# Kernel tuning notes

Measured on AMD Instinct MI355X. Metric: run time of the kernel, lower is better.

The kernel has to match this reference:

```python
import jax, jax.numpy as jnp
import numpy as np

B, S, T = 32, 32, 64          # docs, sentences/doc, tokens/sentence
E, HW, HS = 128, 128, 128     # embed, word hidden, sentence hidden
CW, CS = 128, 128             # attention context sizes
V, NC = 50000, 8              # vocab, classes


def setup_inputs() -> dict:
    key = jax.random.key(0)
    ks = iter(jax.random.split(key, 40))
    x = jax.random.randint(next(ks), (B, S, T), 1, V, dtype=jnp.int32)
    wl = jax.random.randint(next(ks), (B, S), 8, T + 1)   # word lengths
    sl = jax.random.randint(next(ks), (B,), 8, S + 1)     # sentence counts
    tmask = jnp.arange(T)[None, None, :] < wl[:, :, None]
    smask = (jnp.arange(S)[None, :] < sl[:, None])[:, :, None]
    x = jnp.where(tmask & smask, x, 0)                     # 0 = pad token

    def u(shape, scale=0.1):
        return jax.random.uniform(next(ks), shape, jnp.float32, -scale, scale)

    d = {"x": x, "emb": u((V, E))}
    # GRU params in torch layout: W_ih [3H,D] (r|z|n), W_hh [3H,H], biases [3H]
    for pre, Din, H in [("wf", E, HW), ("wb", E, HW), ("sf", 2 * HW, HS), ("sb", 2 * HW, HS)]:
        d[pre + "_Wih"] = u((3 * H, Din))
        d[pre + "_Whh"] = u((3 * H, H))
        d[pre + "_bih"] = u((3 * H,))
        d[pre + "_bhh"] = u((3 * H,))
    d["wproj_W"] = u((CW, 2 * HW)); d["wproj_b"] = u((CW,)); d["wctx"] = u((CW,))
    d["sproj_W"] = u((CS, 2 * HS)); d["sproj_b"] = u((CS,)); d["sctx"] = u((CS,))
    d["fc_W"] = u((NC, 2 * HS)); d["fc_b"] = u((NC,))
    return d


def seq_lens_2d(tok):
    # torch get_sequence_lens: T - trailing zeros, 1 if all zero
    nz = tok != 0
    any_nz = jnp.any(nz, axis=1)
    last = tok.shape[1] - jnp.argmax(nz[:, ::-1], axis=1)
    return jnp.where(any_nz, last, 1)


def doc_lens(x):
    # torch get_num_sentences_lens: S - trailing all-zero sentences
    nz = jnp.any(x != 0, axis=2)  # [B,S]
    any_nz = jnp.any(nz, axis=1)
    last = x.shape[1] - jnp.argmax(nz[:, ::-1], axis=1)
    return jnp.where(any_nz, last, 1)


def run_gru(x, lens, Wih, Whh, bih, bhh, reverse):
    # x: [N,Tm,D]; emulates pack_padded: state frozen / output zeroed beyond len
    N, Tm, _ = x.shape
    H = Whh.shape[1]
    xp = jnp.einsum('ntd,gd->ntg', x, Wih) + bih  # [N,Tm,3H]

    def step(h, inp):
        xg, t = inp
        hg = h @ Whh.T + bhh
        xr, xz, xn = jnp.split(xg, 3, axis=-1)
        hr, hz, hn = jnp.split(hg, 3, axis=-1)
        r = jax.nn.sigmoid(xr + hr)
        z = jax.nn.sigmoid(xz + hz)
        n = jnp.tanh(xn + r * hn)
        h_new = (1 - z) * n + z * h
        valid = (t < lens)[:, None]
        h_new = jnp.where(valid, h_new, h)
        return h_new, jnp.where(valid, h_new, 0.0)

    h0 = jnp.zeros((N, H), x.dtype)
    _, ys = jax.lax.scan(step, h0, (jnp.swapaxes(xp, 0, 1), jnp.arange(Tm)), reverse=reverse)
    return jnp.swapaxes(ys, 0, 1)  # [N,Tm,H]


def bigru(x, lens, pf, pb):
    return jnp.concatenate([run_gru(x, lens, *pf, reverse=False),
                            run_gru(x, lens, *pb, reverse=True)], axis=-1)


def attn_pool(out, lens, Wp, bp, ctx):
    # faithful to torch: softmax over padded positions up to max(lens)
    # (pad_packed pads to max length; padded outputs are zero but score=tanh(b)@c)
    Tm = out.shape[1]
    scores = jnp.tanh(out @ Wp.T + bp) @ ctx            # [N,Tm]
    valid = jnp.arange(Tm)[None, :] < jnp.max(lens)
    attn = jax.nn.softmax(jnp.where(valid, scores, -jnp.inf), axis=-1)
    return jnp.einsum('nt,nth->nh', attn, out)


def han_forward(x, emb,
                wf_Wih, wf_Whh, wf_bih, wf_bhh, wb_Wih, wb_Whh, wb_bih, wb_bhh,
                wproj_W, wproj_b, wctx,
                sf_Wih, sf_Whh, sf_bih, sf_bhh, sb_Wih, sb_Whh, sb_bih, sb_bhh,
                sproj_W, sproj_b, sctx, fc_W, fc_b):
    Bx, Sx, Tx = x.shape
    xw = x.reshape(-1, Tx)                      # [B*S, T]
    wlens = seq_lens_2d(xw)
    slens = doc_lens(x)
    we = emb[xw]                                # [B*S, T, E]
    wout = bigru(we, wlens, (wf_Wih, wf_Whh, wf_bih, wf_bhh),
                 (wb_Wih, wb_Whh, wb_bih, wb_bhh))     # [B*S, T, 2HW]
    sent = attn_pool(wout, wlens, wproj_W, wproj_b, wctx)  # [B*S, 2HW]
    sent = sent.reshape(Bx, Sx, -1)
    sout = bigru(sent, slens, (sf_Wih, sf_Whh, sf_bih, sf_bhh),
                 (sb_Wih, sb_Whh, sb_bih, sb_bhh))     # [B, S, 2HS]
    doc = attn_pool(sout, slens, sproj_W, sproj_b, sctx)   # [B, 2HS]
    return doc @ fc_W.T + fc_b                             # [B, NC]


def reference(x, emb,
              wf_Wih, wf_Whh, wf_bih, wf_bhh, wb_Wih, wb_Whh, wb_bih, wb_bhh,
              wproj_W, wproj_b, wctx,
              sf_Wih, sf_Whh, sf_bih, sf_bhh, sb_Wih, sb_Whh, sb_bih, sb_bhh,
              sproj_W, sproj_b, sctx, fc_W, fc_b):
    return han_forward(x, emb,
                       wf_Wih, wf_Whh, wf_bih, wf_bhh, wb_Wih, wb_Whh, wb_bih, wb_bhh,
                       wproj_W, wproj_b, wctx,
                       sf_Wih, sf_Whh, sf_bih, sf_bhh, sb_Wih, sb_Whh, sb_bih, sb_bhh,
                       sproj_W, sproj_b, sctx, fc_W, fc_b)
```

## Files before the change

kernel.cpp:

```cpp
#include <hip/hip_runtime.h>
#include <hip/hip_bf16.h>

typedef unsigned short ushort_t;
typedef __attribute__((ext_vector_type(4))) float floatx4;
typedef __attribute__((ext_vector_type(8))) short short8;

__device__ __forceinline__ float bf2f(ushort_t u) {
    union { unsigned int i; float f; } v; v.i = ((unsigned int)u) << 16; return v.f;
}
__device__ __forceinline__ ushort_t f2bf(float f) {
    union { float f; unsigned int i; } v; v.f = f;
    unsigned int i = v.i;
    i += 0x7fffu + ((i >> 16) & 1u);
    return (ushort_t)(i >> 16);
}
__device__ __forceinline__ float fsig(float x)  { return 1.f / (1.f + __expf(-x)); }
__device__ __forceinline__ float ftanh(float x) { return 1.f - 2.f / (__expf(2.f * x) + 1.f); }

__device__ __forceinline__ floatx4 MFMA16(short8 a, short8 b, floatx4 c) {
    return __builtin_amdgcn_mfma_f32_16x16x32_bf16(a, b, c, 0, 0, 0);
}

#define XIDX(c, m) ((((c) * 16) + ((m) ^ ((c) & 15))) * 8)

__global__ __launch_bounds__(64) void detect_kernel(const unsigned int* __restrict__ raw,
                                                    int* __restrict__ flag,
                                                    int* __restrict__ wmax,
                                                    int* __restrict__ smax) {
    int c = 0;
    for (int i = 0; i < 16; ++i) {
        unsigned int v = raw[threadIdx.x * 16 + i];
        unsigned int e = (v >> 7) & 0xFFu;
        if (e > 0x7Bu) ++c;
    }
    c += __shfl_xor(c, 1);  c += __shfl_xor(c, 2);  c += __shfl_xor(c, 4);
    c += __shfl_xor(c, 8);  c += __shfl_xor(c, 16); c += __shfl_xor(c, 32);
    if (threadIdx.x == 0) {
        *flag = (c > 64) ? 1 : 0;
        *wmax = 0;
        *smax = 0;
    }
}

struct ConvArgs {
    const void* src[25];
    int dstoff[25];
    int count[25];
    int cumblk[26];
};

__global__ __launch_bounds__(256) void convert_kernel(ConvArgs a, ushort_t* __restrict__ dst,
                                                      const int* __restrict__ flag) {
    int b = blockIdx.x;
    int lo = 0, hi = 24;
    while (lo < hi) { int mid = (lo + hi + 1) >> 1; if (a.cumblk[mid] <= b) lo = mid; else hi = mid - 1; }
    int j = lo;
    size_t base = (size_t)(b - a.cumblk[j]) * 2048 + (size_t)threadIdx.x * 8;
    if (base >= (size_t)a.count[j]) return;
    ushort_t* out = dst + a.dstoff[j] + base;
    if (*flag) {
        const float* s = (const float*)a.src[j] + base;
        float4 v0 = *(const float4*)s;
        float4 v1 = *(const float4*)(s + 4);
        union { ushort_t u[8]; uint4 v; } o;
        o.u[0] = f2bf(v0.x); o.u[1] = f2bf(v0.y); o.u[2] = f2bf(v0.z); o.u[3] = f2bf(v0.w);
        o.u[4] = f2bf(v1.x); o.u[5] = f2bf(v1.y); o.u[6] = f2bf(v1.z); o.u[7] = f2bf(v1.w);
        *(uint4*)out = o.v;
    } else {
        *(uint4*)out = *(const uint4*)((const ushort_t*)a.src[j] + base);
    }
}

__global__ __launch_bounds__(64) void lens_kernel(const int* __restrict__ x,
                                                  int* wlens, int* slens,
                                                  int* wmax, int* smax) {
    int b = blockIdx.x, s = threadIdx.x;
    int last = 0;
    if (s < 32) {
        const int* tok = x + (b * 32 + s) * 64;
        for (int t = 0; t < 64; t += 4) {
            int4 v = *(const int4*)(tok + t);
            if (v.x) last = t + 1;
            if (v.y) last = t + 2;
            if (v.z) last = t + 3;
            if (v.w) last = t + 4;
        }
        wlens[b * 32 + s] = last ? last : 1;
    }
    int len = (s < 32) ? (last ? last : 1) : 0;
    int lm = len;
    for (int off = 32; off; off >>= 1) lm = max(lm, __shfl_xor(lm, off));
    unsigned long long mask = __ballot(s < 32 && last > 0);
    if (s == 0) {
        int sl = mask ? (63 - (int)__clzll(mask) + 1) : 1;
        slens[b] = sl;
        atomicMax(smax, sl);
        atomicMax(wmax, lm);
    }
}

__global__ __launch_bounds__(512, 2) void word_gru_kernel(
        const int* __restrict__ x, const ushort_t* __restrict__ emb,
        const ushort_t* __restrict__ Wih_f, const ushort_t* __restrict__ Whh_f,
        const ushort_t* __restrict__ bih_f, const ushort_t* __restrict__ bhh_f,
        const ushort_t* __restrict__ Wih_b, const ushort_t* __restrict__ Whh_b,
        const ushort_t* __restrict__ bih_b, const ushort_t* __restrict__ bhh_b,
        const int* __restrict__ lens, ushort_t* __restrict__ out) {
    const int T = 64;
    __shared__ ushort_t h_buf[2][2048];
    __shared__ ushort_t x_buf[2][2048];
    __shared__ float bsum_lds[256];
    __shared__ float bihn_lds[128];
    __shared__ float bhhn_lds[128];
    __shared__ int tok_lds[1024];

    int tid = threadIdx.x;
    int d = blockIdx.y;
    int n0 = blockIdx.x * 16;
    const ushort_t* Wih = d ? Wih_b : Wih_f;
    const ushort_t* Whh = d ? Whh_b : Whh_f;
    const ushort_t* bih = d ? bih_b : bih_f;
    const ushort_t* bhh = d ? bhh_b : bhh_f;
    int lane = tid & 63, wave = tid >> 6;
    int l15 = lane & 15, l4 = (lane >> 4) & 3;
    int jt = wave * 16;
    int j0 = jt + l4 * 4;

    ((int2*)tok_lds)[tid] = ((const int2*)(x + n0 * 64))[tid];
    if (tid < 256) bsum_lds[tid] = bf2f(bih[tid]) + bf2f(bhh[tid]);
    else if (tid < 384) {
        bihn_lds[tid - 256] = bf2f(bih[tid]);
        bhhn_lds[tid - 256] = bf2f(bhh[tid]);
    }
    { uint2 z = {0u, 0u}; *(uint2*)&h_buf[0][tid * 4] = z; }

    short8 wr[4], wz[4], wn[4], ur[4], uz[4], un[4];
    #pragma unroll
    for (int kf = 0; kf < 4; ++kf) {
        int col = kf * 32 + l4 * 8;
        wr[kf] = *(const short8*)(Wih + (size_t)(jt + l15) * 128 + col);
        wz[kf] = *(const short8*)(Wih + (size_t)(128 + jt + l15) * 128 + col);
        wn[kf] = *(const short8*)(Wih + (size_t)(256 + jt + l15) * 128 + col);
        ur[kf] = *(const short8*)(Whh + (size_t)(jt + l15) * 128 + col);
        uz[kf] = *(const short8*)(Whh + (size_t)(128 + jt + l15) * 128 + col);
        un[kf] = *(const short8*)(Whh + (size_t)(256 + jt + l15) * 128 + col);
    }
    __syncthreads();

    floatx4 br  = *(floatx4*)&bsum_lds[j0];
    floatx4 bz  = *(floatx4*)&bsum_lds[128 + j0];
    floatx4 bxn = *(floatx4*)&bihn_lds[j0];
    floatx4 bhn = *(floatx4*)&bhhn_lds[j0];
    int lv = lens[n0 + l15];
    float hreg[4] = {0.f, 0.f, 0.f, 0.f};

    int m_s = tid >> 4, c_s = tid & 15;
    if (tid < 256) {
        int t0 = d ? (T - 1) : 0;
        int tok = tok_lds[m_s * 64 + t0];
        uint4 v = *(const uint4*)(emb + (size_t)tok * 128 + c_s * 8);
        *(uint4*)&x_buf[0][XIDX(c_s, m_s)] = v;
    }
    __syncthreads();

    for (int ti = 0; ti < T; ++ti) {
        int t = d ? (T - 1 - ti) : ti;
        int cur = ti & 1;
        uint4 xnext;
        bool have_next = (ti + 1) < T;
        if (tid < 256 && have_next) {
            int tn = d ? (T - 2 - ti) : (ti + 1);
            xnext = *(const uint4*)(emb + (size_t)tok_lds[m_s * 64 + tn] * 128 + c_s * 8);
        }
        floatx4 ar = br, az = bz, axn = bxn, ahn = bhn;
        #pragma unroll
        for (int kf = 0; kf < 4; ++kf) {
            short8 xb = *(const short8*)&x_buf[cur][XIDX(kf * 4 + l4, l15)];
            short8 hb = *(const short8*)&h_buf[cur][XIDX(kf * 4 + l4, l15)];
            ar  = MFMA16(wr[kf], xb, ar);
            ar  = MFMA16(ur[kf], hb, ar);
            az  = MFMA16(wz[kf], xb, az);
            az  = MFMA16(uz[kf], hb, az);
            axn = MFMA16(wn[kf], xb, axn);
            ahn = MFMA16(un[kf], hb, ahn);
        }
        bool valid = t < lv;
        ushort_t hu[4], ou[4];
        #pragma unroll
        for (int i = 0; i < 4; ++i) {
            float r  = fsig(ar[i]);
            float z  = fsig(az[i]);
            float nn = ftanh(axn[i] + r * ahn[i]);
            float hv = valid ? (nn + z * (hreg[i] - nn)) : hreg[i];
            hreg[i] = hv;
            hu[i] = f2bf(hv);
            ou[i] = valid ? hu[i] : (ushort_t)0;
        }
        ushort4 h4; h4.x = hu[0]; h4.y = hu[1]; h4.z = hu[2]; h4.w = hu[3];
        ushort4 o4; o4.x = ou[0]; o4.y = ou[1]; o4.z = ou[2]; o4.w = ou[3];
        *(ushort4*)&h_buf[cur ^ 1][XIDX(j0 >> 3, l15) + (j0 & 7)] = h4;
        *(ushort4*)(out + ((size_t)(n0 + l15) * T + t) * 256 + d * 128 + j0) = o4;
        if (tid < 256 && have_next)
            *(uint4*)&x_buf[cur ^ 1][XIDX(c_s, m_s)] = xnext;
        __syncthreads();
    }
}

__global__ __launch_bounds__(512, 1) void sent_gru_kernel(
        const ushort_t* __restrict__ sent,
        const ushort_t* __restrict__ Wih_f, const ushort_t* __restrict__ Whh_f,
        const ushort_t* __restrict__ bih_f, const ushort_t* __restrict__ bhh_f,
        const ushort_t* __restrict__ Wih_b, const ushort_t* __restrict__ Whh_b,
        const ushort_t* __restrict__ bih_b, const ushort_t* __restrict__ bhh_b,
        const int* __restrict__ lens, ushort_t* __restrict__ out) {
    const int T = 32;
    __shared__ ushort_t h_buf[2][2048];
    __shared__ ushort_t x_buf[2][4096];
    __shared__ float bsum_lds[256];
    __shared__ float bihn_lds[128];
    __shared__ float bhhn_lds[128];

    int tid = threadIdx.x;
    int d = blockIdx.y;
    int n0 = blockIdx.x * 16;
    const ushort_t* Wih = d ? Wih_b : Wih_f;
    const ushort_t* Whh = d ? Whh_b : Whh_f;
    const ushort_t* bih = d ? bih_b : bih_f;
    const ushort_t* bhh = d ? bhh_b : bhh_f;
    int lane = tid & 63, wave = tid >> 6;
    int l15 = lane & 15, l4 = (lane >> 4) & 3;
    int jt = wave * 16;
    int j0 = jt + l4 * 4;

    if (tid < 256) bsum_lds[tid] = bf2f(bih[tid]) + bf2f(bhh[tid]);
    else if (tid < 384) {
        bihn_lds[tid - 256] = bf2f(bih[tid]);
        bhhn_lds[tid - 256] = bf2f(bhh[tid]);
    }
    { uint2 z = {0u, 0u}; *(uint2*)&h_buf[0][tid * 4] = z; }

    short8 wr[8], wz[8], wn[8];
    #pragma unroll
    for (int kf = 0; kf < 8; ++kf) {
        int col = kf * 32 + l4 * 8;
        wr[kf] = *(const short8*)(Wih + (size_t)(jt + l15) * 256 + col);
        wz[kf] = *(const short8*)(Wih + (size_t)(128 + jt + l15) * 256 + col);
        wn[kf] = *(const short8*)(Wih + (size_t)(256 + jt + l15) * 256 + col);
    }
    short8 ur[4], uz[4], un[4];
    #pragma unroll
    for (int kf = 0; kf < 4; ++kf) {
        int col = kf * 32 + l4 * 8;
        ur[kf] = *(const short8*)(Whh + (size_t)(jt + l15) * 128 + col);
        uz[kf] = *(const short8*)(Whh + (size_t)(128 + jt + l15) * 128 + col);
        un[kf] = *(const short8*)(Whh + (size_t)(256 + jt + l15) * 128 + col);
    }
    __syncthreads();

    floatx4 br  = *(floatx4*)&bsum_lds[j0];
    floatx4 bz  = *(floatx4*)&bsum_lds[128 + j0];
    floatx4 bxn = *(floatx4*)&bihn_lds[j0];
    floatx4 bhn = *(floatx4*)&bhhn_lds[j0];
    int lv = lens[n0 + l15];
    float hreg[4] = {0.f, 0.f, 0.f, 0.f};

    int m_x = tid >> 5, c_x = tid & 31;
    {
        int t0 = d ? (T - 1) : 0;
        uint4 v = *(const uint4*)(sent + ((size_t)(n0 + m_x) * T + t0) * 256 + c_x * 8);
        *(uint4*)&x_buf[0][XIDX(c_x, m_x)] = v;
    }
    __syncthreads();

    for (int ti = 0; ti < T; ++ti) {
        int t = d ? (T - 1 - ti) : ti;
        int cur = ti & 1;
        uint4 xnext;
        bool have_next = (ti + 1) < T;
        if (have_next) {
            int tn = d ? (T - 2 - ti) : (ti + 1);
            xnext = *(const uint4*)(sent + ((size_t)(n0 + m_x) * T + tn) * 256 + c_x * 8);
        }
        floatx4 ar = br, az = bz, axn = bxn, ahn = bhn;
        #pragma unroll
        for (int kf = 0; kf < 8; ++kf) {
            short8 xb = *(const short8*)&x_buf[cur][XIDX(kf * 4 + l4, l15)];
            ar  = MFMA16(wr[kf], xb, ar);
            az  = MFMA16(wz[kf], xb, az);
            axn = MFMA16(wn[kf], xb, axn);
        }
        #pragma unroll
        for (int kf = 0; kf < 4; ++kf) {
            short8 hb = *(const short8*)&h_buf[cur][XIDX(kf * 4 + l4, l15)];
            ar  = MFMA16(ur[kf], hb, ar);
            az  = MFMA16(uz[kf], hb, az);
            ahn = MFMA16(un[kf], hb, ahn);
        }
        bool valid = t < lv;
        ushort_t hu[4], ou[4];
        #pragma unroll
        for (int i = 0; i < 4; ++i) {
            float r  = fsig(ar[i]);
            float z  = fsig(az[i]);
            float nn = ftanh(axn[i] + r * ahn[i]);
            float hv = valid ? (nn + z * (hreg[i] - nn)) : hreg[i];
            hreg[i] = hv;
            hu[i] = f2bf(hv);
            ou[i] = valid ? hu[i] : (ushort_t)0;
        }
        ushort4 h4; h4.x = hu[0]; h4.y = hu[1]; h4.z = hu[2]; h4.w = hu[3];
        ushort4 o4; o4.x = ou[0]; o4.y = ou[1]; o4.z = ou[2]; o4.w = ou[3];
        *(ushort4*)&h_buf[cur ^ 1][XIDX(j0 >> 3, l15) + (j0 & 7)] = h4;
        *(ushort4*)(out + ((size_t)(n0 + l15) * T + t) * 256 + d * 128 + j0) = o4;
        if (have_next)
            *(uint4*)&x_buf[cur ^ 1][XIDX(c_x, m_x)] = xnext;
        __syncthreads();
    }
}

#define SP 264
__global__ __launch_bounds__(256) void word_attn_kernel(const ushort_t* __restrict__ wout,
                                                        const ushort_t* __restrict__ W,
                                                        const ushort_t* __restrict__ bias,
                                                        const ushort_t* __restrict__ ctx,
                                                        const int* __restrict__ maxptr,
                                                        ushort_t* __restrict__ sent) {
    __shared__ ushort_t tile[64 * SP];
    __shared__ float bc[256];
    __shared__ float sc_lds[64];
    __shared__ float p_lds[64];
    int tid = threadIdx.x, g = blockIdx.x;
    for (int idx = tid; idx < 2048; idx += 256) {
        int row = idx >> 5, k0 = (idx & 31) * 8;
        *(uint4*)&tile[row * SP + k0] = *(const uint4*)(wout + ((size_t)g * 64 + row) * 256 + k0);
    }
    if (tid < 128) bc[tid] = bf2f(bias[tid]);
    else bc[tid] = bf2f(ctx[tid - 128]);
    __syncthreads();
    int lane = tid & 63, wave = tid >> 6;
    int l15 = lane & 15, l4 = (lane >> 4) & 3;
    short8 a[8];
    #pragma unroll
    for (int kf = 0; kf < 8; ++kf)
        a[kf] = *(const short8*)&tile[(wave * 16 + l15) * SP + kf * 32 + l4 * 8];
    floatx4 acc[8];
    #pragma unroll
    for (int nt = 0; nt < 8; ++nt) {
        floatx4 c = {0.f, 0.f, 0.f, 0.f};
        #pragma unroll
        for (int kf = 0; kf < 8; ++kf) {
            short8 b = *(const short8*)(W + (size_t)(nt * 16 + l15) * 256 + kf * 32 + l4 * 8);
            c = MFMA16(a[kf], b, c);
        }
        acc[nt] = c;
    }
    float s[4] = {0.f, 0.f, 0.f, 0.f};
    #pragma unroll
    for (int nt = 0; nt < 8; ++nt) {
        float bv = bc[nt * 16 + l15], cv = bc[128 + nt * 16 + l15];
        #pragma unroll
        for (int i = 0; i < 4; ++i)
            s[i] += ftanh(acc[nt][i] + bv) * cv;
    }
    #pragma unroll
    for (int i = 0; i < 4; ++i) {
        s[i] += __shfl_xor(s[i], 1);
        s[i] += __shfl_xor(s[i], 2);
        s[i] += __shfl_xor(s[i], 4);
        s[i] += __shfl_xor(s[i], 8);
    }
    if (l15 == 0) {
        #pragma unroll
        for (int i = 0; i < 4; ++i) sc_lds[wave * 16 + l4 * 4 + i] = s[i];
    }
    __syncthreads();
    if (tid < 64) {
        int ml = *maxptr;
        bool v = tid < ml;
        float sc = v ? sc_lds[tid] : -1e30f;
        float mx = sc;
        for (int off = 32; off; off >>= 1) mx = fmaxf(mx, __shfl_xor(mx, off));
        float e = v ? __expf(sc - mx) : 0.f;
        float sum = e;
        for (int off = 32; off; off >>= 1) sum += __shfl_xor(sum, off);
        p_lds[tid] = e / fmaxf(sum, 1e-30f);
    }
    __syncthreads();
    float acc2 = 0.f;
    for (int t = 0; t < 64; ++t) acc2 += p_lds[t] * bf2f(tile[t * SP + tid]);
    sent[(size_t)g * 256 + tid] = f2bf(acc2);
}

__global__ __launch_bounds__(256) void sent_attn_fc_kernel(const ushort_t* __restrict__ sout,
                                                           const ushort_t* __restrict__ W,
                                                           const ushort_t* __restrict__ bias,
                                                           const ushort_t* __restrict__ ctx,
                                                           const ushort_t* __restrict__ fcW,
                                                           const ushort_t* __restrict__ fcb,
                                                           const int* __restrict__ maxptr,
                                                           const int* __restrict__ flagp,
                                                           void* __restrict__ outp) {
    __shared__ ushort_t tile[32 * SP];
    __shared__ float bc[256];
    __shared__ float sc_lds[32];
    __shared__ float p_lds[32];
    __shared__ float dv[256];
    int tid = threadIdx.x, g = blockIdx.x;
    for (int idx = tid; idx < 1024; idx += 256) {
        int row = idx >> 5, k0 = (idx & 31) * 8;
        *(uint4*)&tile[row * SP + k0] = *(const uint4*)(sout + ((size_t)g * 32 + row) * 256 + k0);
    }
    if (tid < 128) bc[tid] = bf2f(bias[tid]);
    else bc[tid] = bf2f(ctx[tid - 128]);
    __syncthreads();
    int lane = tid & 63, wave = tid >> 6;
    int l15 = lane & 15, l4 = (lane >> 4) & 3;
    if (wave < 2) {
        short8 a[8];
        #pragma unroll
        for (int kf = 0; kf < 8; ++kf)
            a[kf] = *(const short8*)&tile[(wave * 16 + l15) * SP + kf * 32 + l4 * 8];
        floatx4 acc[8];
        #pragma unroll
        for (int nt = 0; nt < 8; ++nt) {
            floatx4 c = {0.f, 0.f, 0.f, 0.f};
            #pragma unroll
            for (int kf = 0; kf < 8; ++kf) {
                short8 b = *(const short8*)(W + (size_t)(nt * 16 + l15) * 256 + kf * 32 + l4 * 8);
                c = MFMA16(a[kf], b, c);
            }
            acc[nt] = c;
        }
        float s[4] = {0.f, 0.f, 0.f, 0.f};
        #pragma unroll
        for (int nt = 0; nt < 8; ++nt) {
            float bv = bc[nt * 16 + l15], cv = bc[128 + nt * 16 + l15];
            #pragma unroll
            for (int i = 0; i < 4; ++i)
                s[i] += ftanh(acc[nt][i] + bv) * cv;
        }
        #pragma unroll
        for (int i = 0; i < 4; ++i) {
            s[i] += __shfl_xor(s[i], 1);
            s[i] += __shfl_xor(s[i], 2);
            s[i] += __shfl_xor(s[i], 4);
            s[i] += __shfl_xor(s[i], 8);
        }
        if (l15 == 0) {
            #pragma unroll
            for (int i = 0; i < 4; ++i) sc_lds[wave * 16 + l4 * 4 + i] = s[i];
        }
    }
    __syncthreads();
    if (tid < 32) {
        int ml = *maxptr;
        bool v = tid < ml;
        float sc = v ? sc_lds[tid] : -1e30f;
        float mx = sc;
        for (int off = 16; off; off >>= 1) mx = fmaxf(mx, __shfl_xor(mx, off));
        float e = v ? __expf(sc - mx) : 0.f;
        float sum = e;
        for (int off = 16; off; off >>= 1) sum += __shfl_xor(sum, off);
        p_lds[tid] = e / fmaxf(sum, 1e-30f);
    }
    __syncthreads();
    float acc2 = 0.f;
    for (int t = 0; t < 32; ++t) acc2 += p_lds[t] * bf2f(tile[t * SP + tid]);
    dv[tid] = acc2;
    __syncthreads();
    int c = tid >> 5, q0 = (tid & 31) * 8;
    float partial = 0.f;
    #pragma unroll
    for (int q = 0; q < 8; ++q)
        partial += dv[q0 + q] * bf2f(fcW[(size_t)c * 256 + q0 + q]);
    for (int off = 16; off; off >>= 1) partial += __shfl_xor(partial, off);
    if ((tid & 31) == 0) {
        float v = partial + bf2f(fcb[c]);
        if (*flagp) ((float*)outp)[g * 8 + c] = v;
        else        ((ushort_t*)outp)[g * 8 + c] = f2bf(v);
    }
}

extern "C" void kernel_launch(void* const* d_in, const int* in_sizes, int n_in,
                              void* d_out, int out_size, void* d_ws, size_t ws_size,
                              hipStream_t stream) {
    const int* x = (const int*)d_in[0];
    char* ws = (char*)d_ws;

    const size_t O_CONV = 0;
    const size_t O_WOUT = 14680064;
    const size_t O_SENT = 48234496;
    const size_t O_SOUT = 48758784;
    const size_t O_LENS = 49283072;
    const size_t O_SLEN = 49287168;
    const size_t O_WMAX = 49287296;
    const size_t O_SMAX = 49287300;
    const size_t O_FLAG = 49287304;

    ushort_t* conv = (ushort_t*)(ws + O_CONV);
    ushort_t* wout = (ushort_t*)(ws + O_WOUT);
    ushort_t* sent = (ushort_t*)(ws + O_SENT);
    ushort_t* sout = (ushort_t*)(ws + O_SOUT);
    int* wlens = (int*)(ws + O_LENS);
    int* slens = (int*)(ws + O_SLEN);
    int* wmax  = (int*)(ws + O_WMAX);
    int* smax  = (int*)(ws + O_SMAX);
    int* flag  = (int*)(ws + O_FLAG);

    ConvArgs ca;
    ushort_t* cw[25];
    int off = 0, blk = 0;
    for (int i = 1; i <= 25; ++i) {
        int j = i - 1;
        int cnt = in_sizes[i];
        ca.src[j] = d_in[i];
        ca.dstoff[j] = off;
        ca.count[j] = cnt;
        ca.cumblk[j] = blk;
        cw[j] = conv + off;
        off += cnt;
        blk += (cnt + 2047) / 2048;
    }
    ca.cumblk[25] = blk;

    detect_kernel<<<1, 64, 0, stream>>>((const unsigned int*)d_in[1], flag, wmax, smax);
    convert_kernel<<<blk, 256, 0, stream>>>(ca, conv, flag);
    lens_kernel<<<32, 64, 0, stream>>>(x, wlens, slens, wmax, smax);
    word_gru_kernel<<<dim3(64, 2), 512, 0, stream>>>(
        x, cw[0],
        cw[1], cw[2], cw[3], cw[4],
        cw[5], cw[6], cw[7], cw[8],
        wlens, wout);
    word_attn_kernel<<<1024, 256, 0, stream>>>(wout, cw[17], cw[18], cw[19], wmax, sent);
    sent_gru_kernel<<<dim3(2, 2), 512, 0, stream>>>(
        sent,
        cw[9], cw[10], cw[11], cw[12],
        cw[13], cw[14], cw[15], cw[16],
        slens, sout);
    sent_attn_fc_kernel<<<32, 256, 0, stream>>>(sout, cw[20], cw[21], cw[22],
                                                cw[23], cw[24], smax, flag, d_out);
    (void)n_in; (void)out_size; (void)ws_size;
}
```

Measured before the change: 322.0 us.

## Merge detect into lens kernel, split GRU accumulators, use LDS-only barriers

```diff
diff --git a/kernel.cpp b/kernel.cpp
--- a/kernel.cpp
+++ b/kernel.cpp
@@ -21,24 +21,49 @@
     return __builtin_amdgcn_mfma_f32_16x16x32_bf16(a, b, c, 0, 0, 0);
 }
 
+__device__ __forceinline__ void bar_lds() {
+    asm volatile("s_waitcnt lgkmcnt(0)" ::: "memory");
+    __builtin_amdgcn_s_barrier();
+}
+
 #define XIDX(c, m) ((((c) * 16) + ((m) ^ ((c) & 15))) * 8)
 
-__global__ __launch_bounds__(64) void detect_kernel(const unsigned int* __restrict__ raw,
-                                                    int* __restrict__ flag,
-                                                    int* __restrict__ wmax,
-                                                    int* __restrict__ smax) {
-    int c = 0;
-    for (int i = 0; i < 16; ++i) {
-        unsigned int v = raw[threadIdx.x * 16 + i];
-        unsigned int e = (v >> 7) & 0xFFu;
-        if (e > 0x7Bu) ++c;
-    }
-    c += __shfl_xor(c, 1);  c += __shfl_xor(c, 2);  c += __shfl_xor(c, 4);
-    c += __shfl_xor(c, 8);  c += __shfl_xor(c, 16); c += __shfl_xor(c, 32);
-    if (threadIdx.x == 0) {
-        *flag = (c > 64) ? 1 : 0;
-        *wmax = 0;
-        *smax = 0;
+__global__ __launch_bounds__(64) void lens_kernel(const int* __restrict__ x,
+                                                  const unsigned int* __restrict__ raw,
+                                                  int* wlens, int* slens, int* dmax,
+                                                  int* flag) {
+    int b = blockIdx.x, s = threadIdx.x;
+    if (b == 32) {
+        int c = 0;
+        for (int i = 0; i < 16; ++i) {
+            unsigned int v = raw[s * 16 + i];
+            unsigned int e = (v >> 7) & 0xFFu;
+            if (e > 0x7Bu) ++c;
+        }
+        c += __shfl_xor(c, 1);  c += __shfl_xor(c, 2);  c += __shfl_xor(c, 4);
+        c += __shfl_xor(c, 8);  c += __shfl_xor(c, 16); c += __shfl_xor(c, 32);
+        if (s == 0) *flag = (c > 64) ? 1 : 0;
+        return;
+    }
+    int last = 0;
+    if (s < 32) {
+        const int* tok = x + (b * 32 + s) * 64;
+        for (int t = 0; t < 64; t += 4) {
+            int4 v = *(const int4*)(tok + t);
+            if (v.x) last = t + 1;
+            if (v.y) last = t + 2;
+            if (v.z) last = t + 3;
+            if (v.w) last = t + 4;
+        }
+        wlens[b * 32 + s] = last ? last : 1;
+    }
+    int len = (s < 32) ? (last ? last : 1) : 0;
+    int lm = len;
+    for (int off = 32; off; off >>= 1) lm = max(lm, __shfl_xor(lm, off));
+    unsigned long long mask = __ballot(s < 32 && last > 0);
+    if (s == 0) {
+        slens[b] = mask ? (63 - (int)__clzll(mask) + 1) : 1;
+        dmax[b] = lm;
     }
 }
 
@@ -71,34 +96,6 @@
     }
 }
 
-__global__ __launch_bounds__(64) void lens_kernel(const int* __restrict__ x,
-                                                  int* wlens, int* slens,
-                                                  int* wmax, int* smax) {
-    int b = blockIdx.x, s = threadIdx.x;
-    int last = 0;
-    if (s < 32) {
-        const int* tok = x + (b * 32 + s) * 64;
-        for (int t = 0; t < 64; t += 4) {
-            int4 v = *(const int4*)(tok + t);
-            if (v.x) last = t + 1;
-            if (v.y) last = t + 2;
-            if (v.z) last = t + 3;
-            if (v.w) last = t + 4;
-        }
-        wlens[b * 32 + s] = last ? last : 1;
-    }
-    int len = (s < 32) ? (last ? last : 1) : 0;
-    int lm = len;
-    for (int off = 32; off; off >>= 1) lm = max(lm, __shfl_xor(lm, off));
-    unsigned long long mask = __ballot(s < 32 && last > 0);
-    if (s == 0) {
-        int sl = mask ? (63 - (int)__clzll(mask) + 1) : 1;
-        slens[b] = sl;
-        atomicMax(smax, sl);
-        atomicMax(wmax, lm);
-    }
-}
-
 __global__ __launch_bounds__(512, 2) void word_gru_kernel(
         const int* __restrict__ x, const ushort_t* __restrict__ emb,
         const ushort_t* __restrict__ Wih_f, const ushort_t* __restrict__ Whh_f,
@@ -172,24 +169,32 @@
             int tn = d ? (T - 2 - ti) : (ti + 1);
             xnext = *(const uint4*)(emb + (size_t)tok_lds[m_s * 64 + tn] * 128 + c_s * 8);
         }
-        floatx4 ar = br, az = bz, axn = bxn, ahn = bhn;
+        short8 xb[4], hb[4];
         #pragma unroll
         for (int kf = 0; kf < 4; ++kf) {
-            short8 xb = *(const short8*)&x_buf[cur][XIDX(kf * 4 + l4, l15)];
-            short8 hb = *(const short8*)&h_buf[cur][XIDX(kf * 4 + l4, l15)];
-            ar  = MFMA16(wr[kf], xb, ar);
-            ar  = MFMA16(ur[kf], hb, ar);
-            az  = MFMA16(wz[kf], xb, az);
-            az  = MFMA16(uz[kf], hb, az);
-            axn = MFMA16(wn[kf], xb, axn);
-            ahn = MFMA16(un[kf], hb, ahn);
+            xb[kf] = *(const short8*)&x_buf[cur][XIDX(kf * 4 + l4, l15)];
+            hb[kf] = *(const short8*)&h_buf[cur][XIDX(kf * 4 + l4, l15)];
+        }
+        floatx4 arx = br, azx = bz, axn = bxn;
+        floatx4 arh = {0.f, 0.f, 0.f, 0.f}, azh = {0.f, 0.f, 0.f, 0.f}, ahn = bhn;
+        #pragma unroll
+        for (int kf = 0; kf < 4; ++kf) {
+            arx = MFMA16(wr[kf], xb[kf], arx);
+            azx = MFMA16(wz[kf], xb[kf], azx);
+            axn = MFMA16(wn[kf], xb[kf], axn);
+        }
+        #pragma unroll
+        for (int kf = 0; kf < 4; ++kf) {
+            arh = MFMA16(ur[kf], hb[kf], arh);
+            azh = MFMA16(uz[kf], hb[kf], azh);
+            ahn = MFMA16(un[kf], hb[kf], ahn);
         }
         bool valid = t < lv;
         ushort_t hu[4], ou[4];
         #pragma unroll
         for (int i = 0; i < 4; ++i) {
-            float r  = fsig(ar[i]);
-            float z  = fsig(az[i]);
+            float r  = fsig(arx[i] + arh[i]);
+            float z  = fsig(azx[i] + azh[i]);
             float nn = ftanh(axn[i] + r * ahn[i]);
             float hv = valid ? (nn + z * (hreg[i] - nn)) : hreg[i];
             hreg[i] = hv;
@@ -202,7 +207,7 @@
         *(ushort4*)(out + ((size_t)(n0 + l15) * T + t) * 256 + d * 128 + j0) = o4;
         if (tid < 256 && have_next)
             *(uint4*)&x_buf[cur ^ 1][XIDX(c_s, m_s)] = xnext;
-        __syncthreads();
+        bar_lds();
     }
 }
 
@@ -281,27 +286,28 @@
             int tn = d ? (T - 2 - ti) : (ti + 1);
             xnext = *(const uint4*)(sent + ((size_t)(n0 + m_x) * T + tn) * 256 + c_x * 8);
         }
-        floatx4 ar = br, az = bz, axn = bxn, ahn = bhn;
+        floatx4 arx = br, azx = bz, axn = bxn;
+        floatx4 arh = {0.f, 0.f, 0.f, 0.f}, azh = {0.f, 0.f, 0.f, 0.f}, ahn = bhn;
         #pragma unroll
         for (int kf = 0; kf < 8; ++kf) {
             short8 xb = *(const short8*)&x_buf[cur][XIDX(kf * 4 + l4, l15)];
-            ar  = MFMA16(wr[kf], xb, ar);
-            az  = MFMA16(wz[kf], xb, az);
+            arx = MFMA16(wr[kf], xb, arx);
+            azx = MFMA16(wz[kf], xb, azx);
             axn = MFMA16(wn[kf], xb, axn);
         }
         #pragma unroll
         for (int kf = 0; kf < 4; ++kf) {
             short8 hb = *(const short8*)&h_buf[cur][XIDX(kf * 4 + l4, l15)];
-            ar  = MFMA16(ur[kf], hb, ar);
-            az  = MFMA16(uz[kf], hb, az);
+            arh = MFMA16(ur[kf], hb, arh);
+            azh = MFMA16(uz[kf], hb, azh);
             ahn = MFMA16(un[kf], hb, ahn);
         }
         bool valid = t < lv;
         ushort_t hu[4], ou[4];
         #pragma unroll
         for (int i = 0; i < 4; ++i) {
-            float r  = fsig(ar[i]);
-            float z  = fsig(az[i]);
+            float r  = fsig(arx[i] + arh[i]);
+            float z  = fsig(azx[i] + azh[i]);
             float nn = ftanh(axn[i] + r * ahn[i]);
             float hv = valid ? (nn + z * (hreg[i] - nn)) : hreg[i];
             hreg[i] = hv;
@@ -314,7 +320,7 @@
         *(ushort4*)(out + ((size_t)(n0 + l15) * T + t) * 256 + d * 128 + j0) = o4;
         if (have_next)
             *(uint4*)&x_buf[cur ^ 1][XIDX(c_x, m_x)] = xnext;
-        __syncthreads();
+        bar_lds();
     }
 }
 
@@ -323,7 +329,7 @@
                                                         const ushort_t* __restrict__ W,
                                                         const ushort_t* __restrict__ bias,
                                                         const ushort_t* __restrict__ ctx,
-                                                        const int* __restrict__ maxptr,
+                                                        const int* __restrict__ dmax,
                                                         ushort_t* __restrict__ sent) {
     __shared__ ushort_t tile[64 * SP];
     __shared__ float bc[256];
@@ -375,7 +381,8 @@
     }
     __syncthreads();
     if (tid < 64) {
-        int ml = *maxptr;
+        int ml = dmax[tid & 31];
+        for (int off = 32; off; off >>= 1) ml = max(ml, __shfl_xor(ml, off));
         bool v = tid < ml;
         float sc = v ? sc_lds[tid] : -1e30f;
         float mx = sc;
@@ -397,7 +404,7 @@
                                                            const ushort_t* __restrict__ ctx,
                                                            const ushort_t* __restrict__ fcW,
                                                            const ushort_t* __restrict__ fcb,
-                                                           const int* __restrict__ maxptr,
+                                                           const int* __restrict__ slens,
                                                            const int* __restrict__ flagp,
                                                            void* __restrict__ outp) {
     __shared__ ushort_t tile[32 * SP];
@@ -453,14 +460,15 @@
     }
     __syncthreads();
     if (tid < 32) {
-        int ml = *maxptr;
+        int ml = slens[tid];
+        for (int off = 16; off; off >>= 1) ml = max(ml, __shfl_xor(ml, off, 32));
         bool v = tid < ml;
         float sc = v ? sc_lds[tid] : -1e30f;
         float mx = sc;
-        for (int off = 16; off; off >>= 1) mx = fmaxf(mx, __shfl_xor(mx, off));
+        for (int off = 16; off; off >>= 1) mx = fmaxf(mx, __shfl_xor(mx, off, 32));
         float e = v ? __expf(sc - mx) : 0.f;
         float sum = e;
-        for (int off = 16; off; off >>= 1) sum += __shfl_xor(sum, off);
+        for (int off = 16; off; off >>= 1) sum += __shfl_xor(sum, off, 32);
         p_lds[tid] = e / fmaxf(sum, 1e-30f);
     }
     __syncthreads();
@@ -473,7 +481,7 @@
     #pragma unroll
     for (int q = 0; q < 8; ++q)
         partial += dv[q0 + q] * bf2f(fcW[(size_t)c * 256 + q0 + q]);
-    for (int off = 16; off; off >>= 1) partial += __shfl_xor(partial, off);
+    for (int off = 16; off; off >>= 1) partial += __shfl_xor(partial, off, 32);
     if ((tid & 31) == 0) {
         float v = partial + bf2f(fcb[c]);
         if (*flagp) ((float*)outp)[g * 8 + c] = v;
@@ -493,9 +501,8 @@
     const size_t O_SOUT = 48758784;
     const size_t O_LENS = 49283072;
     const size_t O_SLEN = 49287168;
-    const size_t O_WMAX = 49287296;
-    const size_t O_SMAX = 49287300;
-    const size_t O_FLAG = 49287304;
+    const size_t O_DMAX = 49287296;
+    const size_t O_FLAG = 49287424;
 
     ushort_t* conv = (ushort_t*)(ws + O_CONV);
     ushort_t* wout = (ushort_t*)(ws + O_WOUT);
@@ -503,8 +510,7 @@
     ushort_t* sout = (ushort_t*)(ws + O_SOUT);
     int* wlens = (int*)(ws + O_LENS);
     int* slens = (int*)(ws + O_SLEN);
-    int* wmax  = (int*)(ws + O_WMAX);
-    int* smax  = (int*)(ws + O_SMAX);
+    int* dmax  = (int*)(ws + O_DMAX);
     int* flag  = (int*)(ws + O_FLAG);
 
     ConvArgs ca;
@@ -523,21 +529,21 @@
     }
     ca.cumblk[25] = blk;
 
-    detect_kernel<<<1, 64, 0, stream>>>((const unsigned int*)d_in[1], flag, wmax, smax);
+    lens_kernel<<<33, 64, 0, stream>>>(x, (const unsigned int*)d_in[1],
+                                       wlens, slens, dmax, flag);
     convert_kernel<<<blk, 256, 0, stream>>>(ca, conv, flag);
-    lens_kernel<<<32, 64, 0, stream>>>(x, wlens, slens, wmax, smax);
     word_gru_kernel<<<dim3(64, 2), 512, 0, stream>>>(
         x, cw[0],
         cw[1], cw[2], cw[3], cw[4],
         cw[5], cw[6], cw[7], cw[8],
         wlens, wout);
-    word_attn_kernel<<<1024, 256, 0, stream>>>(wout, cw[17], cw[18], cw[19], wmax, sent);
+    word_attn_kernel<<<1024, 256, 0, stream>>>(wout, cw[17], cw[18], cw[19], dmax, sent);
     sent_gru_kernel<<<dim3(2, 2), 512, 0, stream>>>(
         sent,
         cw[9], cw[10], cw[11], cw[12],
         cw[13], cw[14], cw[15], cw[16],
         slens, sout);
     sent_attn_fc_kernel<<<32, 256, 0, stream>>>(sout, cw[20], cw[21], cw[22],
-                                                cw[23], cw[24], smax, flag, d_out);
+                                                cw[23], cw[24], slens, flag, d_out);
     (void)n_in; (void)out_size; (void)ws_size;
 }
```

Measured after the change: 322.6 us. No clear change (+0.2%).
